# Kernel optimization log

Hardware: AMD Instinct MI355X
Metric: run time of the kernel (lower is better)

## Reference

```python
import jax, jax.numpy as jnp
import numpy as np

B, T, D, H = 64, 512, 512, 512


def setup_inputs() -> dict:
    key = jax.random.key(0)
    k1, k2, k3, k4 = jax.random.split(key, 4)
    return {
        "x": jax.random.normal(k1, (B, T, D), dtype=jnp.float32),
        "kernel": jax.random.normal(k2, (D, 4 * H), dtype=jnp.float32) * 0.02,
        "recurrent_kernel": jax.random.normal(k3, (H, 4 * H), dtype=jnp.float32) * 0.02,
        "bias": jax.random.normal(k4, (4 * H,), dtype=jnp.float32) * 0.02,
    }


def reference(x, kernel, recurrent_kernel, bias):
    # Faithful MyLSTM forward, return_sequences=True.
    # tf.split order along last axis: i, f, c, o.
    b = x.shape[0]
    h0 = jnp.zeros((b, H), dtype=x.dtype)
    c0 = jnp.zeros((b, H), dtype=x.dtype)
    xs = jnp.swapaxes(x, 0, 1)  # [T, B, D]

    def step(carry, xt):
        h, c = carry
        # fused gate GEMM; mathematically identical to the 4 separate matmuls
        z = xt @ kernel + h @ recurrent_kernel + bias  # [B, 4H]
        i_t = jax.nn.sigmoid(z[:, 0 * H:1 * H])
        f_t = jax.nn.sigmoid(z[:, 1 * H:2 * H])
        c_tilde = jnp.tanh(z[:, 2 * H:3 * H])
        o_t = jax.nn.sigmoid(z[:, 3 * H:4 * H])
        # NB: module applies tanh to c_t and carries the ACTIVATED cell state
        c_new = jnp.tanh(f_t * c + i_t * c_tilde)
        h_new = o_t * c_new
        return (h_new, c_new), h_new

    (_, _), hs = jax.lax.scan(step, (h0, c0), xs)
    return jnp.swapaxes(hs, 0, 1)  # [B, T, H]
```

## Files before the change

### kernel.cpp

```cpp
#include <hip/hip_runtime.h>
#include <hip/hip_bf16.h>
#include <stdint.h>


#define Bdim 64
#define Tdim 512
#define Ddim 512
#define Hdim 512
#define G4H  2048
#define NG 4
#define NS 32
#define BH (Bdim * Hdim)

typedef __bf16 bf16_t;
typedef __bf16 bf16x8 __attribute__((ext_vector_type(8)));
typedef float  f32x4  __attribute__((ext_vector_type(4)));
typedef uint32_t u32x4 __attribute__((ext_vector_type(4)));
union pv128 { u32x4 u; f32x4 f; bf16x8 h; };
union bu16 { bf16_t b; unsigned short u; };

__device__ __forceinline__ float sigmoid_f(float x) {
  return 1.0f / (1.0f + __expf(-x));
}
__device__ __forceinline__ float tanh_f(float x) {
  return 1.0f - 2.0f / (__expf(2.0f * x) + 1.0f);
}

__global__ void transpose_bf16_512x2048(const float* __restrict__ src,
                                        bf16_t* __restrict__ dst) {
  __shared__ bf16_t tile[64][72];
  int c0 = blockIdx.x * 64;
  int r0 = blockIdx.y * 64;
  int tx = threadIdx.x & 63;
  int ty = threadIdx.x >> 6;
#pragma unroll
  for (int i = 0; i < 64; i += 4)
    tile[ty + i][tx] = (bf16_t)src[(size_t)(r0 + ty + i) * G4H + c0 + tx];
  __syncthreads();
#pragma unroll
  for (int i = 0; i < 64; i += 4)
    dst[(size_t)(c0 + ty + i) * Ddim + r0 + tx] = tile[tx][ty + i];
}

__global__ void cast_bf16(const float* __restrict__ in, bf16_t* __restrict__ out) {
  size_t i = ((size_t)blockIdx.x * blockDim.x + threadIdx.x) * 8;
  f32x4 a = *(const f32x4*)(in + i);
  f32x4 b = *(const f32x4*)(in + i + 4);
  bf16x8 v;
#pragma unroll
  for (int j = 0; j < 4; ++j) { v[j] = (bf16_t)a[j]; v[j + 4] = (bf16_t)b[j]; }
  *(bf16x8*)(out + i) = v;
}

#define MFMA16(A, B, C) __builtin_amdgcn_mfma_f32_16x16x32_bf16(A, B, C, 0, 0, 0)

#define ISSUE_POLL()                                                         \
  asm volatile(                                                              \
      "global_load_dwordx4 %0, %8, off sc0 sc1\n\t"                          \
      "global_load_dwordx4 %1, %8, off offset:16 sc0 sc1\n\t"                \
      "global_load_dwordx4 %2, %8, off offset:128 sc0 sc1\n\t"               \
      "global_load_dwordx4 %3, %8, off offset:144 sc0 sc1\n\t"               \
      "global_load_dwordx4 %4, %8, off offset:256 sc0 sc1\n\t"               \
      "global_load_dwordx4 %5, %8, off offset:272 sc0 sc1\n\t"               \
      "global_load_dwordx4 %6, %8, off offset:384 sc0 sc1\n\t"               \
      "global_load_dwordx4 %7, %8, off offset:400 sc0 sc1"                   \
      : "=v"(p0.f), "=v"(p1.f), "=v"(p2.f), "=v"(p3.f), "=v"(p4.f),          \
        "=v"(p5.f), "=v"(p6.f), "=v"(p7.f)                                   \
      : "v"(hb)                                                              \
      : "memory")

#define CHECK(P)                                                             \
  do {                                                                       \
    bad |= (P.u[0] ^ st) & 15u;                                              \
    bad |= (P.u[1] ^ st) & 15u;                                              \
    bad |= (P.u[2] ^ st) & 15u;                                              \
    bad |= (P.u[3] ^ st) & 15u;                                              \
  } while (0)

#define HU(PA, PB, c)                                                        \
  do {                                                                       \
    pv128 hi_, lo_;                                                          \
    hi_.u[0] = (PA.u[0] >> 16) | (PA.u[1] & 0xFFFF0000u);                    \
    hi_.u[1] = (PA.u[2] >> 16) | (PA.u[3] & 0xFFFF0000u);                    \
    hi_.u[2] = (PB.u[0] >> 16) | (PB.u[1] & 0xFFFF0000u);                    \
    hi_.u[3] = (PB.u[2] >> 16) | (PB.u[3] & 0xFFFF0000u);                    \
    lo_.u[0] = (PA.u[0] & 0xFFF0u) | ((PA.u[1] & 0xFFF0u) << 16);            \
    lo_.u[1] = (PA.u[2] & 0xFFF0u) | ((PA.u[3] & 0xFFF0u) << 16);            \
    lo_.u[2] = (PB.u[0] & 0xFFF0u) | ((PB.u[1] & 0xFFF0u) << 16);            \
    lo_.u[3] = (PB.u[2] & 0xFFF0u) | ((PB.u[3] & 0xFFF0u) << 16);            \
    a0 = MFMA16(hi_.h, Ur[0][c], a0);                                        \
    a1 = MFMA16(hi_.h, Ur[1][c], a1);                                        \
    a2 = MFMA16(hi_.h, Ur[2][c], a2);                                        \
    a3 = MFMA16(hi_.h, Ur[3][c], a3);                                        \
    a0 = MFMA16(lo_.h, Ur[0][c], a0);                                        \
    a1 = MFMA16(lo_.h, Ur[1][c], a1);                                        \
    a2 = MFMA16(lo_.h, Ur[2][c], a2);                                        \
    a3 = MFMA16(lo_.h, Ur[3][c], a3);                                        \
  } while (0)

__launch_bounds__(256, 1)
__global__ void lstm_fused(const bf16_t* __restrict__ xb,
                           const bf16_t* __restrict__ Wt,
                           const bf16_t* __restrict__ Ut,
                           const float* __restrict__ bias,
                           float* __restrict__ out,
                           uint32_t* __restrict__ hbuf) {
  __shared__ float EX[4][4][16][17];

  const int blk  = blockIdx.x;
  const int g    = blk >> 5;
  const int s    = blk & 31;
  const int wv   = threadIdx.x >> 6;
  const int lane = threadIdx.x & 63;
  const int l15  = lane & 15;
  const int l4   = lane >> 4;
  const int b0   = g * 16;
  const int hc0  = s * 16;
  const int k0   = wv * 128;

  bf16x8 Wr[4][4], Ur[4][4];
#pragma unroll
  for (int G = 0; G < 4; ++G) {
    const bf16_t* wsrc = Wt + (size_t)(G * Hdim + hc0 + l15) * Ddim + k0 + l4 * 8;
    const bf16_t* usrc = Ut + (size_t)(G * Hdim + hc0 + l15) * Ddim + k0 + l4 * 8;
#pragma unroll
    for (int c = 0; c < 4; ++c) {
      Wr[G][c] = *(const bf16x8*)(wsrc + c * 32);
      Ur[G][c] = *(const bf16x8*)(usrc + c * 32);
    }
  }

  const int urow = threadIdx.x >> 4;
  const int ucol = threadIdx.x & 15;
  float b4[4];
#pragma unroll
  for (int G = 0; G < 4; ++G) b4[G] = bias[G * Hdim + hc0 + ucol];
  float cstate = 0.f;
  float* outp = out + (size_t)(b0 + urow) * Tdim * Hdim + hc0 + ucol;
  uint32_t* hpub = hbuf + (size_t)(b0 + urow) * Hdim + hc0 + ucol;
  const uint32_t* hrd = hbuf + (size_t)(b0 + l15) * Hdim + k0 + l4 * 8;
  const bf16_t* xrow = xb + (size_t)(b0 + l15) * Tdim * Ddim + l4 * 8 + k0;

  pv128 xr0, xr1, xr2, xr3;
  asm volatile(
      "global_load_dwordx4 %0, %4, off\n\t"
      "global_load_dwordx4 %1, %4, off offset:64\n\t"
      "global_load_dwordx4 %2, %4, off offset:128\n\t"
      "global_load_dwordx4 %3, %4, off offset:192\n\t"
      "s_waitcnt vmcnt(0)"
      : "=v"(xr0.f), "=v"(xr1.f), "=v"(xr2.f), "=v"(xr3.f)
      : "v"(xrow) : "memory");
  __builtin_amdgcn_sched_barrier(0);

  bool dead = false;

  for (int t = 0; t < Tdim; ++t) {
    pv128 p0, p1, p2, p3, p4, p5, p6, p7;
    const uint32_t st = (uint32_t)t & 15u;
    const uint32_t* hb = hrd + (((t - 1) & 1) ? BH : 0);

    if (t > 0 && !dead) {
      ISSUE_POLL();
      __builtin_amdgcn_sched_barrier(0);
    }

    f32x4 a0 = {0, 0, 0, 0}, a1 = {0, 0, 0, 0}, a2 = {0, 0, 0, 0}, a3 = {0, 0, 0, 0};
#define XW(c, xv)                                                            \
    a0 = MFMA16(xv.h, Wr[0][c], a0);                                         \
    a1 = MFMA16(xv.h, Wr[1][c], a1);                                         \
    a2 = MFMA16(xv.h, Wr[2][c], a2);                                         \
    a3 = MFMA16(xv.h, Wr[3][c], a3);
    XW(0, xr0) XW(1, xr1) XW(2, xr2) XW(3, xr3)
#undef XW

    if (t > 0) {
      if (!dead) {
        int guard = 0;
        for (;;) {
          asm volatile("s_waitcnt vmcnt(0)" ::: "memory");
          __builtin_amdgcn_sched_barrier(0);
          uint32_t bad = 0;
          CHECK(p0); CHECK(p1); CHECK(p2); CHECK(p3);
          CHECK(p4); CHECK(p5); CHECK(p6); CHECK(p7);
          if (__all(bad == 0)) break;
          if (++guard > 200000) { dead = true; break; }
          ISSUE_POLL();
          __builtin_amdgcn_sched_barrier(0);
        }
      } else {
        p0.u = p1.u = p2.u = p3.u = p4.u = p5.u = p6.u = p7.u = (u32x4)(0u);
      }
      HU(p0, p1, 0);
      HU(p2, p3, 1);
      HU(p4, p5, 2);
      HU(p6, p7, 3);
    }

    {
      const bf16_t* xp = xrow + (size_t)((t + 1 < Tdim) ? t + 1 : Tdim - 1) * Ddim;
      asm volatile(
          "global_load_dwordx4 %0, %4, off\n\t"
          "global_load_dwordx4 %1, %4, off offset:64\n\t"
          "global_load_dwordx4 %2, %4, off offset:128\n\t"
          "global_load_dwordx4 %3, %4, off offset:192"
          : "=v"(xr0.f), "=v"(xr1.f), "=v"(xr2.f), "=v"(xr3.f)
          : "v"(xp) : "memory");
    }

#pragma unroll
    for (int G = 0; G < 4; ++G) {
      f32x4 av = (G == 0) ? a0 : (G == 1) ? a1 : (G == 2) ? a2 : a3;
#pragma unroll
      for (int r = 0; r < 4; ++r) EX[wv][G][l4 * 4 + r][l15] = av[r];
    }
    __syncthreads();

    float z0 = EX[0][0][urow][ucol] + EX[1][0][urow][ucol] +
               EX[2][0][urow][ucol] + EX[3][0][urow][ucol] + b4[0];
    float z1 = EX[0][1][urow][ucol] + EX[1][1][urow][ucol] +
               EX[2][1][urow][ucol] + EX[3][1][urow][ucol] + b4[1];
    float z2 = EX[0][2][urow][ucol] + EX[1][2][urow][ucol] +
               EX[2][2][urow][ucol] + EX[3][2][urow][ucol] + b4[2];
    float z3 = EX[0][3][urow][ucol] + EX[1][3][urow][ucol] +
               EX[2][3][urow][ucol] + EX[3][3][urow][ucol] + b4[3];
    float ig = sigmoid_f(z0), fg = sigmoid_f(z1);
    float ct = tanh_f(z2), og = sigmoid_f(z3);
    float cn = tanh_f(fg * cstate + ig * ct);
    cstate = cn;
    float h = og * cn;

    bu16 hh; hh.b = (bf16_t)h;
    bu16 hl; hl.b = (bf16_t)(h - (float)hh.b);
    uint32_t pubw = ((uint32_t)hh.u << 16) | ((uint32_t)hl.u & 0xFFF0u) |
                    ((uint32_t)(t + 1) & 15u);
    uint32_t* dst = hpub + ((t & 1) ? BH : 0);
    asm volatile("global_store_dword %0, %1, off sc0 sc1" ::"v"(dst), "v"(pubw)
                 : "memory");
    __builtin_nontemporal_store(h, outp + (size_t)t * Hdim);

    __syncthreads();

    asm volatile("s_waitcnt vmcnt(0)" ::: "memory");
    __builtin_amdgcn_sched_barrier(0);
  }
}

extern "C" void kernel_launch(void* const* d_in, const int* in_sizes, int n_in,
                              void* d_out, int out_size, void* d_ws, size_t ws_size,
                              hipStream_t stream) {
  const float* x    = (const float*)d_in[0];
  const float* W    = (const float*)d_in[1];
  const float* U    = (const float*)d_in[2];
  const float* bias = (const float*)d_in[3];
  float* out = (float*)d_out;

  unsigned char* ws = (unsigned char*)d_ws;
  uint32_t* hbuf = (uint32_t*)ws;
  bf16_t* Wt = (bf16_t*)(ws + 262144);
  bf16_t* Ut = Wt + (size_t)G4H * Ddim;
  bf16_t* xb = Ut + (size_t)G4H * Ddim;

  hipMemsetAsync(hbuf, 0, 262144, stream);

  cast_bf16<<<(Bdim * Tdim * Ddim) / 2048, 256, 0, stream>>>(x, xb);

  dim3 tgrid(G4H / 64, Ddim / 64);
  transpose_bf16_512x2048<<<tgrid, 256, 0, stream>>>(W, Wt);
  transpose_bf16_512x2048<<<tgrid, 256, 0, stream>>>(U, Ut);

  lstm_fused<<<NG * NS, 256, 0, stream>>>(xb, Wt, Ut, bias, out, hbuf);
}
```

Baseline: 1.468 ms.

## Halve LSTM block count using 8 waves per block over wider hidden slices

Restructures the persistent LSTM kernel from 128 blocks of 4 waves to 64 blocks of 8 waves. Each block now owns 32 hidden columns instead of 16, and each wave covers a 64-wide K slice instead of 128. The intent is to cut the number of blocks that take part in the per-step cross-block h exchange and to shorten each wave's serial MFMA chain. In exchange there are fewer CUs in use, the cross-wave LDS reduction grows from 4 to 8 partials, and there are 8 accumulators per wave.

```diff
diff --git a/kernel.cpp b/kernel.cpp
--- a/kernel.cpp
+++ b/kernel.cpp
@@ -9,7 +9,7 @@
 #define Hdim 512
 #define G4H  2048
 #define NG 4
-#define NS 32
+#define NS 16
 #define BH (Bdim * Hdim)
 
 typedef __bf16 bf16_t;
@@ -56,16 +56,11 @@
 
 #define ISSUE_POLL()                                                         \
   asm volatile(                                                              \
-      "global_load_dwordx4 %0, %8, off sc0 sc1\n\t"                          \
-      "global_load_dwordx4 %1, %8, off offset:16 sc0 sc1\n\t"                \
-      "global_load_dwordx4 %2, %8, off offset:128 sc0 sc1\n\t"               \
-      "global_load_dwordx4 %3, %8, off offset:144 sc0 sc1\n\t"               \
-      "global_load_dwordx4 %4, %8, off offset:256 sc0 sc1\n\t"               \
-      "global_load_dwordx4 %5, %8, off offset:272 sc0 sc1\n\t"               \
-      "global_load_dwordx4 %6, %8, off offset:384 sc0 sc1\n\t"               \
-      "global_load_dwordx4 %7, %8, off offset:400 sc0 sc1"                   \
-      : "=v"(p0.f), "=v"(p1.f), "=v"(p2.f), "=v"(p3.f), "=v"(p4.f),          \
-        "=v"(p5.f), "=v"(p6.f), "=v"(p7.f)                                   \
+      "global_load_dwordx4 %0, %4, off sc0 sc1\n\t"                          \
+      "global_load_dwordx4 %1, %4, off offset:16 sc0 sc1\n\t"                \
+      "global_load_dwordx4 %2, %4, off offset:128 sc0 sc1\n\t"               \
+      "global_load_dwordx4 %3, %4, off offset:144 sc0 sc1"                   \
+      : "=v"(p0.f), "=v"(p1.f), "=v"(p2.f), "=v"(p3.f)                       \
       : "v"(hb)                                                              \
       : "memory")
 
@@ -76,6 +71,16 @@
     bad |= (P.u[2] ^ st) & 15u;                                              \
     bad |= (P.u[3] ^ st) & 15u;                                              \
   } while (0)
+
+#define MM8(AV, WU, c)                                                       \
+  a0 = MFMA16(AV, WU[0][c], a0);                                             \
+  a1 = MFMA16(AV, WU[1][c], a1);                                             \
+  a2 = MFMA16(AV, WU[2][c], a2);                                             \
+  a3 = MFMA16(AV, WU[3][c], a3);                                             \
+  a4 = MFMA16(AV, WU[4][c], a4);                                             \
+  a5 = MFMA16(AV, WU[5][c], a5);                                             \
+  a6 = MFMA16(AV, WU[6][c], a6);                                             \
+  a7 = MFMA16(AV, WU[7][c], a7);
 
 #define HU(PA, PB, c)                                                        \
   do {                                                                       \
@@ -88,50 +93,45 @@
     lo_.u[1] = (PA.u[2] & 0xFFF0u) | ((PA.u[3] & 0xFFF0u) << 16);            \
     lo_.u[2] = (PB.u[0] & 0xFFF0u) | ((PB.u[1] & 0xFFF0u) << 16);            \
     lo_.u[3] = (PB.u[2] & 0xFFF0u) | ((PB.u[3] & 0xFFF0u) << 16);            \
-    a0 = MFMA16(hi_.h, Ur[0][c], a0);                                        \
-    a1 = MFMA16(hi_.h, Ur[1][c], a1);                                        \
-    a2 = MFMA16(hi_.h, Ur[2][c], a2);                                        \
-    a3 = MFMA16(hi_.h, Ur[3][c], a3);                                        \
-    a0 = MFMA16(lo_.h, Ur[0][c], a0);                                        \
-    a1 = MFMA16(lo_.h, Ur[1][c], a1);                                        \
-    a2 = MFMA16(lo_.h, Ur[2][c], a2);                                        \
-    a3 = MFMA16(lo_.h, Ur[3][c], a3);                                        \
+    MM8(hi_.h, Ur, c)                                                        \
+    MM8(lo_.h, Ur, c)                                                        \
   } while (0)
 
-__launch_bounds__(256, 1)
+__launch_bounds__(512, 1)
 __global__ void lstm_fused(const bf16_t* __restrict__ xb,
                            const bf16_t* __restrict__ Wt,
                            const bf16_t* __restrict__ Ut,
                            const float* __restrict__ bias,
                            float* __restrict__ out,
                            uint32_t* __restrict__ hbuf) {
-  __shared__ float EX[4][4][16][17];
+  __shared__ float EX[8][4][16][36];
 
   const int blk  = blockIdx.x;
-  const int g    = blk >> 5;
-  const int s    = blk & 31;
+  const int g    = blk >> 4;
+  const int s    = blk & 15;
   const int wv   = threadIdx.x >> 6;
   const int lane = threadIdx.x & 63;
   const int l15  = lane & 15;
   const int l4   = lane >> 4;
   const int b0   = g * 16;
-  const int hc0  = s * 16;
-  const int k0   = wv * 128;
-
-  bf16x8 Wr[4][4], Ur[4][4];
-#pragma unroll
-  for (int G = 0; G < 4; ++G) {
-    const bf16_t* wsrc = Wt + (size_t)(G * Hdim + hc0 + l15) * Ddim + k0 + l4 * 8;
-    const bf16_t* usrc = Ut + (size_t)(G * Hdim + hc0 + l15) * Ddim + k0 + l4 * 8;
-#pragma unroll
-    for (int c = 0; c < 4; ++c) {
-      Wr[G][c] = *(const bf16x8*)(wsrc + c * 32);
-      Ur[G][c] = *(const bf16x8*)(usrc + c * 32);
+  const int hc0  = s * 32;
+  const int k0   = wv * 64;
+
+  bf16x8 Wr[8][2], Ur[8][2];
+#pragma unroll
+  for (int n = 0; n < 8; ++n) {
+    int zc = (n >> 1) * Hdim + hc0 + (n & 1) * 16 + l15;
+    const bf16_t* wsrc = Wt + (size_t)zc * Ddim + k0 + l4 * 8;
+    const bf16_t* usrc = Ut + (size_t)zc * Ddim + k0 + l4 * 8;
+#pragma unroll
+    for (int c = 0; c < 2; ++c) {
+      Wr[n][c] = *(const bf16x8*)(wsrc + c * 32);
+      Ur[n][c] = *(const bf16x8*)(usrc + c * 32);
     }
   }
 
-  const int urow = threadIdx.x >> 4;
-  const int ucol = threadIdx.x & 15;
+  const int urow = threadIdx.x >> 5;
+  const int ucol = threadIdx.x & 31;
   float b4[4];
 #pragma unroll
   for (int G = 0; G < 4; ++G) b4[G] = bias[G * Hdim + hc0 + ucol];
@@ -139,23 +139,21 @@
   float* outp = out + (size_t)(b0 + urow) * Tdim * Hdim + hc0 + ucol;
   uint32_t* hpub = hbuf + (size_t)(b0 + urow) * Hdim + hc0 + ucol;
   const uint32_t* hrd = hbuf + (size_t)(b0 + l15) * Hdim + k0 + l4 * 8;
-  const bf16_t* xrow = xb + (size_t)(b0 + l15) * Tdim * Ddim + l4 * 8 + k0;
-
-  pv128 xr0, xr1, xr2, xr3;
+  const bf16_t* xrow = xb + (size_t)(b0 + l15) * Tdim * Ddim + k0 + l4 * 8;
+
+  pv128 xr0, xr1;
   asm volatile(
-      "global_load_dwordx4 %0, %4, off\n\t"
-      "global_load_dwordx4 %1, %4, off offset:64\n\t"
-      "global_load_dwordx4 %2, %4, off offset:128\n\t"
-      "global_load_dwordx4 %3, %4, off offset:192\n\t"
+      "global_load_dwordx4 %0, %2, off\n\t"
+      "global_load_dwordx4 %1, %2, off offset:64\n\t"
       "s_waitcnt vmcnt(0)"
-      : "=v"(xr0.f), "=v"(xr1.f), "=v"(xr2.f), "=v"(xr3.f)
+      : "=v"(xr0.f), "=v"(xr1.f)
       : "v"(xrow) : "memory");
   __builtin_amdgcn_sched_barrier(0);
 
   bool dead = false;
 
   for (int t = 0; t < Tdim; ++t) {
-    pv128 p0, p1, p2, p3, p4, p5, p6, p7;
+    pv128 p0, p1, p2, p3;
     const uint32_t st = (uint32_t)t & 15u;
     const uint32_t* hb = hrd + (((t - 1) & 1) ? BH : 0);
 
@@ -165,13 +163,9 @@
     }
 
     f32x4 a0 = {0, 0, 0, 0}, a1 = {0, 0, 0, 0}, a2 = {0, 0, 0, 0}, a3 = {0, 0, 0, 0};
-#define XW(c, xv)                                                            \
-    a0 = MFMA16(xv.h, Wr[0][c], a0);                                         \
-    a1 = MFMA16(xv.h, Wr[1][c], a1);                                         \
-    a2 = MFMA16(xv.h, Wr[2][c], a2);                                         \
-    a3 = MFMA16(xv.h, Wr[3][c], a3);
-    XW(0, xr0) XW(1, xr1) XW(2, xr2) XW(3, xr3)
-#undef XW
+    f32x4 a4 = {0, 0, 0, 0}, a5 = {0, 0, 0, 0}, a6 = {0, 0, 0, 0}, a7 = {0, 0, 0, 0};
+    MM8(xr0.h, Wr, 0)
+    MM8(xr1.h, Wr, 1)
 
     if (t > 0) {
       if (!dead) {
@@ -181,48 +175,45 @@
           __builtin_amdgcn_sched_barrier(0);
           uint32_t bad = 0;
           CHECK(p0); CHECK(p1); CHECK(p2); CHECK(p3);
-          CHECK(p4); CHECK(p5); CHECK(p6); CHECK(p7);
           if (__all(bad == 0)) break;
           if (++guard > 200000) { dead = true; break; }
           ISSUE_POLL();
           __builtin_amdgcn_sched_barrier(0);
         }
       } else {
-        p0.u = p1.u = p2.u = p3.u = p4.u = p5.u = p6.u = p7.u = (u32x4)(0u);
+        p0.u = p1.u = p2.u = p3.u = (u32x4)(0u);
       }
       HU(p0, p1, 0);
       HU(p2, p3, 1);
-      HU(p4, p5, 2);
-      HU(p6, p7, 3);
     }
 
     {
       const bf16_t* xp = xrow + (size_t)((t + 1 < Tdim) ? t + 1 : Tdim - 1) * Ddim;
       asm volatile(
-          "global_load_dwordx4 %0, %4, off\n\t"
-          "global_load_dwordx4 %1, %4, off offset:64\n\t"
-          "global_load_dwordx4 %2, %4, off offset:128\n\t"
-          "global_load_dwordx4 %3, %4, off offset:192"
-          : "=v"(xr0.f), "=v"(xr1.f), "=v"(xr2.f), "=v"(xr3.f)
+          "global_load_dwordx4 %0, %2, off\n\t"
+          "global_load_dwordx4 %1, %2, off offset:64"
+          : "=v"(xr0.f), "=v"(xr1.f)
           : "v"(xp) : "memory");
     }
 
 #pragma unroll
-    for (int G = 0; G < 4; ++G) {
-      f32x4 av = (G == 0) ? a0 : (G == 1) ? a1 : (G == 2) ? a2 : a3;
-#pragma unroll
-      for (int r = 0; r < 4; ++r) EX[wv][G][l4 * 4 + r][l15] = av[r];
+    for (int n = 0; n < 8; ++n) {
+      f32x4 av = (n == 0) ? a0 : (n == 1) ? a1 : (n == 2) ? a2 : (n == 3) ? a3
+               : (n == 4) ? a4 : (n == 5) ? a5 : (n == 6) ? a6 : a7;
+#pragma unroll
+      for (int r = 0; r < 4; ++r)
+        EX[wv][n >> 1][l4 * 4 + r][(n & 1) * 16 + l15] = av[r];
     }
     __syncthreads();
 
-    float z0 = EX[0][0][urow][ucol] + EX[1][0][urow][ucol] +
-               EX[2][0][urow][ucol] + EX[3][0][urow][ucol] + b4[0];
-    float z1 = EX[0][1][urow][ucol] + EX[1][1][urow][ucol] +
-               EX[2][1][urow][ucol] + EX[3][1][urow][ucol] + b4[1];
-    float z2 = EX[0][2][urow][ucol] + EX[1][2][urow][ucol] +
-               EX[2][2][urow][ucol] + EX[3][2][urow][ucol] + b4[2];
-    float z3 = EX[0][3][urow][ucol] + EX[1][3][urow][ucol] +
-               EX[2][3][urow][ucol] + EX[3][3][urow][ucol] + b4[3];
+    float z0 = b4[0], z1 = b4[1], z2 = b4[2], z3 = b4[3];
+#pragma unroll
+    for (int w = 0; w < 8; ++w) {
+      z0 += EX[w][0][urow][ucol];
+      z1 += EX[w][1][urow][ucol];
+      z2 += EX[w][2][urow][ucol];
+      z3 += EX[w][3][urow][ucol];
+    }
     float ig = sigmoid_f(z0), fg = sigmoid_f(z1);
     float ct = tanh_f(z2), og = sigmoid_f(z3);
     float cn = tanh_f(fg * cstate + ig * ct);
@@ -268,5 +259,5 @@
   transpose_bf16_512x2048<<<tgrid, 256, 0, stream>>>(W, Wt);
   transpose_bf16_512x2048<<<tgrid, 256, 0, stream>>>(U, Ut);
 
-  lstm_fused<<<NG * NS, 256, 0, stream>>>(xb, Wt, Ut, bias, out, hbuf);
-}
+  lstm_fused<<<NG * NS, 512, 0, stream>>>(xb, Wt, Ut, bias, out, hbuf);
+}
```

New measurement: 1.381 ms. 5.9% less time.
